# Kernel tuning notes

Measured on AMD Instinct MI355X. Metric: run time of the kernel, lower is better.

The kernel has to match this reference:

```python
import jax, jax.numpy as jnp
import numpy as np

N_NODES = 100000
N_EDGES = 1600000
F_IN = 128
HID = 128
N_GRAPHS = 64


def setup_inputs() -> dict:
    key = jax.random.key(0)
    ks = jax.random.split(key, 8)
    s = 1.0 / np.sqrt(HID)
    x = jax.random.normal(ks[0], (N_NODES, F_IN), jnp.float32)
    edge_index = jax.random.randint(ks[1], (2, N_EDGES), 0, N_NODES)
    batch = jnp.sort(jax.random.randint(ks[2], (N_NODES,), 0, N_GRAPHS))
    return {
        "x": x,
        "edge_index": edge_index,
        "batch": batch,
        "W1": jax.random.normal(ks[3], (F_IN, HID), jnp.float32) * s,
        "b1": jnp.zeros((HID,), jnp.float32),
        "W2": jax.random.normal(ks[4], (HID, HID), jnp.float32) * s,
        "b2": jnp.zeros((HID,), jnp.float32),
        "W3": jax.random.normal(ks[5], (HID, HID), jnp.float32) * s,
        "b3": jnp.zeros((HID,), jnp.float32),
        "lin_w": jax.random.normal(ks[6], (HID, 1), jnp.float32) * s,
        "lin_b": jnp.zeros((1,), jnp.float32),
    }


def reference(x, edge_index, batch, W1, b1, W2, b2, W3, b3, lin_w, lin_b):
    N = x.shape[0]
    # GCN normalization with self-loops: D^-1/2 (A+I) D^-1/2, computed once
    loops = jnp.arange(N)
    row = jnp.concatenate([edge_index[0], loops])  # source nodes
    col = jnp.concatenate([edge_index[1], loops])  # target nodes
    deg = jax.ops.segment_sum(jnp.ones_like(col, x.dtype), col, num_segments=N)
    dinv = jnp.where(deg > 0, jax.lax.rsqrt(deg), 0.0)
    norm = dinv[row] * dinv[col]  # [E+N]

    def conv(h, W, b):
        h = h @ W                                   # [N, H] linear transform
        msg = norm[:, None] * h[row]                # gather + scale [E+N, H]
        agg = jax.ops.segment_sum(msg, col, num_segments=N)
        return jax.nn.relu(agg + b)                 # dropout is identity in eval

    h = conv(x, W1, b1)
    h = conv(h, W2, b2)
    h = conv(h, W3, b3)

    # global mean pool per graph
    cnt = jax.ops.segment_sum(jnp.ones((N,), x.dtype), batch, num_segments=N_GRAPHS)
    pooled = jax.ops.segment_sum(h, batch, num_segments=N_GRAPHS) / jnp.maximum(cnt, 1.0)[:, None]
    out = pooled @ lin_w + lin_b  # [G, 1]
    return out.reshape(-1)
```

## Files before the change

### kernel.cpp

```cpp
#include <hip/hip_runtime.h>


typedef __attribute__((ext_vector_type(4))) float f32x4;
typedef __attribute__((ext_vector_type(8))) _Float16 half8;


__device__ __forceinline__ void gemm_f32_body(const float* __restrict__ H,
                                              const _Float16* __restrict__ W16,
                                              const float* __restrict__ dinv,
                                              _Float16* __restrict__ T16,
                                              int N, int bid) {
    const int tid = threadIdx.x;
    const int wv = tid >> 6;
    const int lane = tid & 63;
    const int r0 = bid * 64 + wv * 16;
    const int mrow = lane & 15;
    const int kq = lane >> 4;
    const int grow = r0 + mrow;
    const bool rok = grow < N;

    f32x4 acc[8];
    #pragma unroll
    for (int t = 0; t < 8; ++t) acc[t] = (f32x4){0.f, 0.f, 0.f, 0.f};

    #pragma unroll
    for (int c = 0; c < 4; ++c) {
        half8 a = (half8)(_Float16)0;
        if (rok) {
            const f32x4* Hp = (const f32x4*)(H + (size_t)grow * 128 + c * 32 + kq * 8);
            f32x4 a0 = __builtin_nontemporal_load(Hp);
            f32x4 a1 = __builtin_nontemporal_load(Hp + 1);
            a[0] = (_Float16)a0[0]; a[1] = (_Float16)a0[1];
            a[2] = (_Float16)a0[2]; a[3] = (_Float16)a0[3];
            a[4] = (_Float16)a1[0]; a[5] = (_Float16)a1[1];
            a[6] = (_Float16)a1[2]; a[7] = (_Float16)a1[3];
        }
        #pragma unroll
        for (int t = 0; t < 8; ++t) {
            half8 w = *(const half8*)&W16[(((c * 8 + t) * 64) + lane) * 8];
            acc[t] = __builtin_amdgcn_mfma_f32_16x16x32_f16(a, w, acc[t], 0, 0, 0);
        }
    }
    #pragma unroll
    for (int r = 0; r < 4; ++r) {
        int orow = r0 + kq * 4 + r;
        if (orow < N) {
            float dv = dinv[orow];
            half8 o;
            #pragma unroll
            for (int t = 0; t < 8; ++t) o[t] = (_Float16)(acc[t][r] * dv);
            *(half8*)(T16 + (size_t)orow * 128 + mrow * 8) = o;
        }
    }
}

__global__ __launch_bounds__(256) void prep_kernel(const float* __restrict__ W1,
                                                   const float* __restrict__ W2,
                                                   const float* __restrict__ W3,
                                                   const float* __restrict__ b1,
                                                   const float* __restrict__ b2,
                                                   const float* __restrict__ b3,
                                                   const float* __restrict__ lin_w,
                                                   _Float16* __restrict__ W16,
                                                   float* __restrict__ bperm,
                                                   const int* __restrict__ ei,
                                                   int* __restrict__ bucketCursor,
                                                   int* __restrict__ coarse,
                                                   int E, int N, int cap) {
    __shared__ int hist[256];
    __shared__ int base_s[256];
    __shared__ int lcur[256];
    if (blockIdx.x < 192) {
        int layer = blockIdx.x >> 6;
        const float* W = (layer == 0) ? W1 : (layer == 1) ? W2 : W3;
        _Float16* Wd = W16 + layer * 16384;
        int i = (blockIdx.x & 63) * 256 + threadIdx.x;
        int j = i & 7;
        int l = (i >> 3) & 63;
        int t = (i >> 9) & 7;
        int c = i >> 12;
        int k = c * 32 + (l >> 4) * 8 + j;
        int ksrc = (layer == 0) ? k : ((k & 7) * 16 + (k >> 3));
        int n = t * 16 + (l & 15);
        Wd[i] = (_Float16)W[ksrc * 128 + n];
    } else if (blockIdx.x < 200) {
        int a = blockIdx.x - 192;
        if (a < 4 && threadIdx.x < 128) {
            const float* src = (a == 0) ? b1 : (a == 1) ? b2 : (a == 2) ? b3 : lin_w;
            int p2 = threadIdx.x;
            bperm[a * 128 + p2] = src[(p2 & 7) * 16 + (p2 >> 3)];
        }
    } else {
        const int tid = threadIdx.x;
        const int nb = (N + 511) >> 9;
        for (int i = tid; i < nb; i += 256) { hist[i] = 0; lcur[i] = 0; }
        __syncthreads();
        const int e0 = (blockIdx.x - 200) * 2048 + tid * 8;
        int c[8], r[8];
        if (e0 < E && ((E & 3) == 0) && e0 + 7 < E) {
            int4 cA = *(const int4*)&ei[E + e0];
            int4 cB = *(const int4*)&ei[E + e0 + 4];
            int4 rA = *(const int4*)&ei[e0];
            int4 rB = *(const int4*)&ei[e0 + 4];
            c[0] = cA.x; c[1] = cA.y; c[2] = cA.z; c[3] = cA.w;
            c[4] = cB.x; c[5] = cB.y; c[6] = cB.z; c[7] = cB.w;
            r[0] = rA.x; r[1] = rA.y; r[2] = rA.z; r[3] = rA.w;
            r[4] = rB.x; r[5] = rB.y; r[6] = rB.z; r[7] = rB.w;
        } else {
            #pragma unroll
            for (int j = 0; j < 8; ++j) {
                int e = e0 + j;
                c[j] = (e < E) ? ei[E + e] : -1;
                r[j] = (e < E) ? ei[e] : 0;
            }
        }
        #pragma unroll
        for (int j = 0; j < 8; ++j)
            if (c[j] >= 0) atomicAdd(&hist[c[j] >> 9], 1);
        __syncthreads();
        for (int i = tid; i < nb; i += 256) {
            int h = hist[i];
            base_s[i] = h ? atomicAdd(&bucketCursor[i], h) : 0;
        }
        __syncthreads();
        #pragma unroll
        for (int j = 0; j < 8; ++j) {
            if (c[j] >= 0) {
                int b = c[j] >> 9;
                int pos = base_s[b] + atomicAdd(&lcur[b], 1);
                if (pos < cap)
                    coarse[(size_t)b * cap + pos] =
                        (int)(((unsigned)(c[j] & 511) << 23) | (unsigned)r[j]);
            }
        }
    }
}

__global__ __launch_bounds__(256) void bscan_kernel(int* __restrict__ bucketCursor,
                                                    int* __restrict__ bucketStart,
                                                    int* __restrict__ rowptr,
                                                    int nb, int cap, int N) {
    __shared__ int ts[256];
    const int t = threadIdx.x;
    int v = (t < nb) ? min(bucketCursor[t], cap) : 0;
    ts[t] = v;
    __syncthreads();
    for (int off = 1; off < 256; off <<= 1) {
        int add = (t >= off) ? ts[t - off] : 0;
        __syncthreads();
        ts[t] += add;
        __syncthreads();
    }
    if (t < nb) {
        bucketStart[t] = ts[t] - v;
        bucketCursor[t] = v;
    }
    if (t == nb - 1) rowptr[N] = ts[t];
}

__global__ __launch_bounds__(512) void binfill_kernel(const int* __restrict__ bucketStart,
                                                      const int* __restrict__ bucketCount,
                                                      const int* __restrict__ coarse,
                                                      int* __restrict__ rowptr,
                                                      float* __restrict__ dinv,
                                                      int* __restrict__ edges,
                                                      int N, int cap) {
    const int b = blockIdx.x;
    const int bn = b << 9;
    const int t = threadIdx.x;
    __shared__ int hist[512];
    __shared__ int scn[512];
    const int cnt = bucketCount[b];
    const size_t cbase = (size_t)b * cap;
    hist[t] = 0;
    __syncthreads();
    for (int i = t; i < cnt; i += 512)
        atomicAdd(&hist[((unsigned)coarse[cbase + i]) >> 23], 1);
    __syncthreads();
    const int myCnt = hist[t];
    if (bn + t < N) dinv[bn + t] = 1.0f / sqrtf((float)myCnt + 1.0f);
    scn[t] = myCnt;
    __syncthreads();
    for (int off = 1; off < 512; off <<= 1) {
        int add = (t >= off) ? scn[t - off] : 0;
        __syncthreads();
        scn[t] += add;
        __syncthreads();
    }
    const int rstart = bucketStart[b] + scn[t] - myCnt;
    if (bn + t < N) rowptr[bn + t] = rstart;
    hist[t] = rstart;
    __syncthreads();
    for (int i = t; i < cnt; i += 512) {
        int pk = coarse[cbase + i];
        int slot = atomicAdd(&hist[((unsigned)pk) >> 23], 1);
        edges[slot] = pk & 0x7FFFFF;
    }
}

__global__ __launch_bounds__(256) void gemm1_kernel(const float* __restrict__ x,
                                                    const _Float16* __restrict__ W16,
                                                    const float* __restrict__ dinv,
                                                    _Float16* __restrict__ A16, int N) {
    gemm_f32_body(x, W16, dinv, A16, N, blockIdx.x);
}

__global__ __launch_bounds__(256) void gemm_f16_kernel(const _Float16* __restrict__ H16,
                                                       const _Float16* __restrict__ W16,
                                                       const float* __restrict__ dinv,
                                                       _Float16* __restrict__ T16,
                                                       int N) {
    const int tid = threadIdx.x;
    const int wv = tid >> 6;
    const int lane = tid & 63;
    const int r0 = blockIdx.x * 64 + wv * 16;
    const int mrow = lane & 15;
    const int kq = lane >> 4;
    const int grow = r0 + mrow;
    const bool rok = grow < N;

    f32x4 acc[8];
    #pragma unroll
    for (int t = 0; t < 8; ++t) acc[t] = (f32x4){0.f, 0.f, 0.f, 0.f};

    #pragma unroll
    for (int c = 0; c < 4; ++c) {
        half8 a = (half8)(_Float16)0;
        if (rok) a = *(const half8*)(H16 + (size_t)grow * 128 + c * 32 + kq * 8);
        #pragma unroll
        for (int t = 0; t < 8; ++t) {
            half8 w = *(const half8*)&W16[(((c * 8 + t) * 64) + lane) * 8];
            acc[t] = __builtin_amdgcn_mfma_f32_16x16x32_f16(a, w, acc[t], 0, 0, 0);
        }
    }
    #pragma unroll
    for (int r = 0; r < 4; ++r) {
        int orow = r0 + kq * 4 + r;
        if (orow < N) {
            float dv = dinv[orow];
            half8 o;
            #pragma unroll
            for (int t = 0; t < 8; ++t) o[t] = (_Float16)(acc[t][r] * dv);
            *(half8*)(T16 + (size_t)orow * 128 + mrow * 8) = o;
        }
    }
}

__global__ __launch_bounds__(256) void agg_kernel(const int* __restrict__ rowptr,
                                                  const int* __restrict__ edges,
                                                  const float* __restrict__ dinv,
                                                  const _Float16* __restrict__ A16,
                                                  const float* __restrict__ bias,
                                                  _Float16* __restrict__ H16, int N) {
    int w = (blockIdx.x * 256 + threadIdx.x) >> 6;
    if (w >= N) return;
    const int lane = threadIdx.x & 63;
    const int g = lane >> 4;
    const int q = lane & 15;
    const int beg = rowptr[w];
    const int end = rowptr[w + 1];
    const float dn = dinv[w];
    const half8* A8 = (const half8*)A16;

    int myid = (beg + lane < end) ? edges[beg + lane] : 0;
    half8 sv = (half8)(_Float16)0;
    if (g == 0) sv = A8[(size_t)w * 16 + q];

    float a0 = 0.f, a1 = 0.f, a2 = 0.f, a3 = 0.f;
    float a4 = 0.f, a5 = 0.f, a6 = 0.f, a7 = 0.f;
    for (int base = beg; base < end; base += 16) {
        const int rr = base - beg + g;
        const bool v0 = base + g < end;
        const bool v1 = base + g + 4 < end;
        const bool v2 = base + g + 8 < end;
        const bool v3 = base + g + 12 < end;
        int s0 = __shfl(myid, rr < 64 ? rr : 63);
        int s1 = __shfl(myid, rr + 4 < 64 ? rr + 4 : 63);
        int s2 = __shfl(myid, rr + 8 < 64 ? rr + 8 : 63);
        int s3 = __shfl(myid, rr + 12 < 64 ? rr + 12 : 63);
        if (rr >= 64 && v0) s0 = edges[base + g];
        if (rr + 4 >= 64 && v1) s1 = edges[base + g + 4];
        if (rr + 8 >= 64 && v2) s2 = edges[base + g + 8];
        if (rr + 12 >= 64 && v3) s3 = edges[base + g + 12];
        half8 p0, p1, p2, p3;
        if (v0) p0 = A8[(size_t)s0 * 16 + q];
        if (v1) p1 = A8[(size_t)s1 * 16 + q];
        if (v2) p2 = A8[(size_t)s2 * 16 + q];
        if (v3) p3 = A8[(size_t)s3 * 16 + q];
        if (v0) {
            a0 += (float)p0[0]; a1 += (float)p0[1]; a2 += (float)p0[2]; a3 += (float)p0[3];
            a4 += (float)p0[4]; a5 += (float)p0[5]; a6 += (float)p0[6]; a7 += (float)p0[7];
        }
        if (v1) {
            a0 += (float)p1[0]; a1 += (float)p1[1]; a2 += (float)p1[2]; a3 += (float)p1[3];
            a4 += (float)p1[4]; a5 += (float)p1[5]; a6 += (float)p1[6]; a7 += (float)p1[7];
        }
        if (v2) {
            a0 += (float)p2[0]; a1 += (float)p2[1]; a2 += (float)p2[2]; a3 += (float)p2[3];
            a4 += (float)p2[4]; a5 += (float)p2[5]; a6 += (float)p2[6]; a7 += (float)p2[7];
        }
        if (v3) {
            a0 += (float)p3[0]; a1 += (float)p3[1]; a2 += (float)p3[2]; a3 += (float)p3[3];
            a4 += (float)p3[4]; a5 += (float)p3[5]; a6 += (float)p3[6]; a7 += (float)p3[7];
        }
    }
    a0 += __shfl_xor(a0, 16); a1 += __shfl_xor(a1, 16);
    a2 += __shfl_xor(a2, 16); a3 += __shfl_xor(a3, 16);
    a4 += __shfl_xor(a4, 16); a5 += __shfl_xor(a5, 16);
    a6 += __shfl_xor(a6, 16); a7 += __shfl_xor(a7, 16);
    a0 += __shfl_xor(a0, 32); a1 += __shfl_xor(a1, 32);
    a2 += __shfl_xor(a2, 32); a3 += __shfl_xor(a3, 32);
    a4 += __shfl_xor(a4, 32); a5 += __shfl_xor(a5, 32);
    a6 += __shfl_xor(a6, 32); a7 += __shfl_xor(a7, 32);

    if (g == 0) {
        float4 b0 = ((const float4*)bias)[q * 2];
        float4 b1 = ((const float4*)bias)[q * 2 + 1];
        half8 o;
        o[0] = (_Float16)fmaxf(fmaf(dn, a0 + (float)sv[0], b0.x), 0.f);
        o[1] = (_Float16)fmaxf(fmaf(dn, a1 + (float)sv[1], b0.y), 0.f);
        o[2] = (_Float16)fmaxf(fmaf(dn, a2 + (float)sv[2], b0.z), 0.f);
        o[3] = (_Float16)fmaxf(fmaf(dn, a3 + (float)sv[3], b0.w), 0.f);
        o[4] = (_Float16)fmaxf(fmaf(dn, a4 + (float)sv[4], b1.x), 0.f);
        o[5] = (_Float16)fmaxf(fmaf(dn, a5 + (float)sv[5], b1.y), 0.f);
        o[6] = (_Float16)fmaxf(fmaf(dn, a6 + (float)sv[6], b1.z), 0.f);
        o[7] = (_Float16)fmaxf(fmaf(dn, a7 + (float)sv[7], b1.w), 0.f);
        ((half8*)H16)[(size_t)w * 16 + q] = o;
    }
}

__global__ __launch_bounds__(256) void agg_head_kernel(const int* __restrict__ rowptr,
                                                       const int* __restrict__ edges,
                                                       const float* __restrict__ dinv,
                                                       const _Float16* __restrict__ A16,
                                                       const float* __restrict__ bias,
                                                       const float* __restrict__ lin_w,
                                                       float* __restrict__ nodeval, int N) {
    int w = (blockIdx.x * 256 + threadIdx.x) >> 6;
    if (w >= N) return;
    const int lane = threadIdx.x & 63;
    const int g = lane >> 4;
    const int q = lane & 15;
    const int beg = rowptr[w];
    const int end = rowptr[w + 1];
    const float dn = dinv[w];
    const half8* A8 = (const half8*)A16;

    int myid = (beg + lane < end) ? edges[beg + lane] : 0;
    half8 sv = (half8)(_Float16)0;
    if (g == 0) sv = A8[(size_t)w * 16 + q];

    float a0 = 0.f, a1 = 0.f, a2 = 0.f, a3 = 0.f;
    float a4 = 0.f, a5 = 0.f, a6 = 0.f, a7 = 0.f;
    for (int base = beg; base < end; base += 16) {
        const int rr = base - beg + g;
        const bool v0 = base + g < end;
        const bool v1 = base + g + 4 < end;
        const bool v2 = base + g + 8 < end;
        const bool v3 = base + g + 12 < end;
        int s0 = __shfl(myid, rr < 64 ? rr : 63);
        int s1 = __shfl(myid, rr + 4 < 64 ? rr + 4 : 63);
        int s2 = __shfl(myid, rr + 8 < 64 ? rr + 8 : 63);
        int s3 = __shfl(myid, rr + 12 < 64 ? rr + 12 : 63);
        if (rr >= 64 && v0) s0 = edges[base + g];
        if (rr + 4 >= 64 && v1) s1 = edges[base + g + 4];
        if (rr + 8 >= 64 && v2) s2 = edges[base + g + 8];
        if (rr + 12 >= 64 && v3) s3 = edges[base + g + 12];
        half8 p0, p1, p2, p3;
        if (v0) p0 = A8[(size_t)s0 * 16 + q];
        if (v1) p1 = A8[(size_t)s1 * 16 + q];
        if (v2) p2 = A8[(size_t)s2 * 16 + q];
        if (v3) p3 = A8[(size_t)s3 * 16 + q];
        if (v0) {
            a0 += (float)p0[0]; a1 += (float)p0[1]; a2 += (float)p0[2]; a3 += (float)p0[3];
            a4 += (float)p0[4]; a5 += (float)p0[5]; a6 += (float)p0[6]; a7 += (float)p0[7];
        }
        if (v1) {
            a0 += (float)p1[0]; a1 += (float)p1[1]; a2 += (float)p1[2]; a3 += (float)p1[3];
            a4 += (float)p1[4]; a5 += (float)p1[5]; a6 += (float)p1[6]; a7 += (float)p1[7];
        }
        if (v2) {
            a0 += (float)p2[0]; a1 += (float)p2[1]; a2 += (float)p2[2]; a3 += (float)p2[3];
            a4 += (float)p2[4]; a5 += (float)p2[5]; a6 += (float)p2[6]; a7 += (float)p2[7];
        }
        if (v3) {
            a0 += (float)p3[0]; a1 += (float)p3[1]; a2 += (float)p3[2]; a3 += (float)p3[3];
            a4 += (float)p3[4]; a5 += (float)p3[5]; a6 += (float)p3[6]; a7 += (float)p3[7];
        }
    }
    a0 += __shfl_xor(a0, 16); a1 += __shfl_xor(a1, 16);
    a2 += __shfl_xor(a2, 16); a3 += __shfl_xor(a3, 16);
    a4 += __shfl_xor(a4, 16); a5 += __shfl_xor(a5, 16);
    a6 += __shfl_xor(a6, 16); a7 += __shfl_xor(a7, 16);
    a0 += __shfl_xor(a0, 32); a1 += __shfl_xor(a1, 32);
    a2 += __shfl_xor(a2, 32); a3 += __shfl_xor(a3, 32);
    a4 += __shfl_xor(a4, 32); a5 += __shfl_xor(a5, 32);
    a6 += __shfl_xor(a6, 32); a7 += __shfl_xor(a7, 32);

    if (g == 0) {
        float4 b0 = ((const float4*)bias)[q * 2];
        float4 b1 = ((const float4*)bias)[q * 2 + 1];
        float4 w0 = ((const float4*)lin_w)[q * 2];
        float4 w1 = ((const float4*)lin_w)[q * 2 + 1];
        a0 = fmaf(dn, a0 + (float)sv[0], b0.x);
        a1 = fmaf(dn, a1 + (float)sv[1], b0.y);
        a2 = fmaf(dn, a2 + (float)sv[2], b0.z);
        a3 = fmaf(dn, a3 + (float)sv[3], b0.w);
        a4 = fmaf(dn, a4 + (float)sv[4], b1.x);
        a5 = fmaf(dn, a5 + (float)sv[5], b1.y);
        a6 = fmaf(dn, a6 + (float)sv[6], b1.z);
        a7 = fmaf(dn, a7 + (float)sv[7], b1.w);
        float s = fmaxf(a0, 0.f) * w0.x + fmaxf(a1, 0.f) * w0.y
                + fmaxf(a2, 0.f) * w0.z + fmaxf(a3, 0.f) * w0.w
                + fmaxf(a4, 0.f) * w1.x + fmaxf(a5, 0.f) * w1.y
                + fmaxf(a6, 0.f) * w1.z + fmaxf(a7, 0.f) * w1.w;
        s += __shfl_xor(s, 1);
        s += __shfl_xor(s, 2);
        s += __shfl_xor(s, 4);
        s += __shfl_xor(s, 8);
        if (q == 0) nodeval[w] = s;
    }
}

__device__ __forceinline__ int lower_bound_dev(const int* __restrict__ a, int n, int key) {
    int lo = 0, hi = n;
    while (lo < hi) {
        int mid = (lo + hi) >> 1;
        if (a[mid] < key) lo = mid + 1; else hi = mid;
    }
    return lo;
}

__global__ __launch_bounds__(256) void segreduce_kernel(const float* __restrict__ nodeval,
                                                        const int* __restrict__ batch,
                                                        const float* __restrict__ lin_b,
                                                        float* __restrict__ out, int N) {
    const int g = blockIdx.x;
    const int lo = lower_bound_dev(batch, N, g);
    const int hi = lower_bound_dev(batch, N, g + 1);
    float acc = 0.f;
    for (int n = lo + threadIdx.x; n < hi; n += 256) acc += nodeval[n];
    __shared__ float red[256];
    red[threadIdx.x] = acc;
    __syncthreads();
    for (int s = 128; s > 0; s >>= 1) {
        if (threadIdx.x < s) red[threadIdx.x] += red[threadIdx.x + s];
        __syncthreads();
    }
    if (threadIdx.x == 0) {
        float cnt = (float)(hi - lo);
        out[g] = red[0] / fmaxf(cnt, 1.0f) + lin_b[0];
    }
}

extern "C" void kernel_launch(void* const* d_in, const int* in_sizes, int n_in,
                              void* d_out, int out_size, void* d_ws, size_t ws_size,
                              hipStream_t stream) {
    const float* x     = (const float*)d_in[0];
    const int*   ei    = (const int*)d_in[1];
    const int*   batch = (const int*)d_in[2];
    const float* W1    = (const float*)d_in[3];
    const float* b1    = (const float*)d_in[4];
    const float* W2    = (const float*)d_in[5];
    const float* b2    = (const float*)d_in[6];
    const float* W3    = (const float*)d_in[7];
    const float* b3    = (const float*)d_in[8];
    const float* lin_w = (const float*)d_in[9];
    const float* lin_b = (const float*)d_in[10];
    float* out = (float*)d_out;

    const int N = in_sizes[0] / 128;
    const int E = in_sizes[1] / 2;
    const int nb = (N + 511) >> 9;
    const int cap = (((E + nb - 1) / nb) + 4096 + 3) & ~3;
    const int fBlocks = (E + 2047) / 2048;
    const int gBlocks = (N + 63) / 64;
    const int aBlocks = ((size_t)N * 64 + 255) / 256;

    _Float16* A16    = (_Float16*)d_ws;
    _Float16* H16    = A16 + (size_t)N * 128;
    float* dinv      = (float*)(H16 + (size_t)N * 128);
    int*   rowptr    = (int*)(dinv + N);
    int*   edges     = rowptr + (((size_t)N + 4) & ~(size_t)3);
    int*   coarse    = edges + (((size_t)E + 3) & ~(size_t)3);
    int*   bucketCursor = coarse + (size_t)nb * cap;
    int*   bucketStart  = bucketCursor + 256;
    float* nodeval   = (float*)(bucketStart + 256);
    _Float16* W16    = (_Float16*)(nodeval + N);
    float* bperm     = (float*)(W16 + 3 * 16384);

    hipMemsetAsync(bucketCursor, 0, (size_t)nb * sizeof(int), stream);
    prep_kernel<<<200 + fBlocks, 256, 0, stream>>>(W1, W2, W3, b1, b2, b3, lin_w,
                                                   W16, bperm, ei,
                                                   bucketCursor, coarse, E, N, cap);
    bscan_kernel<<<1, 256, 0, stream>>>(bucketCursor, bucketStart, rowptr, nb, cap, N);
    binfill_kernel<<<nb, 512, 0, stream>>>(bucketStart, bucketCursor, coarse,
                                           rowptr, dinv, edges, N, cap);
    gemm1_kernel<<<gBlocks, 256, 0, stream>>>(x, W16, dinv, A16, N);

    agg_kernel<<<aBlocks, 256, 0, stream>>>(rowptr, edges, dinv, A16, bperm, H16, N);
    gemm_f16_kernel<<<gBlocks, 256, 0, stream>>>(H16, W16 + 16384, dinv, A16, N);
    agg_kernel<<<aBlocks, 256, 0, stream>>>(rowptr, edges, dinv, A16, bperm + 128, H16, N);
    gemm_f16_kernel<<<gBlocks, 256, 0, stream>>>(H16, W16 + 32768, dinv, A16, N);
    agg_head_kernel<<<aBlocks, 256, 0, stream>>>(rowptr, edges, dinv,
                                                 A16, bperm + 256, bperm + 384, nodeval, N);
    segreduce_kernel<<<64, 256, 0, stream>>>(nodeval, batch, lin_b, out, N);
}
```

Measured before the change: 413.2 us.

## Process multiple nodes per wave in aggregation kernels with edge-id prefetch

Result: slower. 439.6 us (+6.4%).

```diff
diff --git a/kernel.cpp b/kernel.cpp
--- a/kernel.cpp
+++ b/kernel.cpp
@@ -3,6 +3,8 @@
 
 typedef __attribute__((ext_vector_type(4))) float f32x4;
 typedef __attribute__((ext_vector_type(8))) _Float16 half8;
+
+#define CNODES 8
 
 
 __device__ __forceinline__ void gemm_f32_body(const float* __restrict__ H,
@@ -252,80 +254,95 @@
                                                   const _Float16* __restrict__ A16,
                                                   const float* __restrict__ bias,
                                                   _Float16* __restrict__ H16, int N) {
-    int w = (blockIdx.x * 256 + threadIdx.x) >> 6;
-    if (w >= N) return;
+    const int wid = (blockIdx.x * 256 + threadIdx.x) >> 6;
+    const int a = wid * CNODES;
+    if (a >= N) return;
     const int lane = threadIdx.x & 63;
     const int g = lane >> 4;
     const int q = lane & 15;
-    const int beg = rowptr[w];
-    const int end = rowptr[w + 1];
-    const float dn = dinv[w];
     const half8* A8 = (const half8*)A16;
 
-    int myid = (beg + lane < end) ? edges[beg + lane] : 0;
-    half8 sv = (half8)(_Float16)0;
-    if (g == 0) sv = A8[(size_t)w * 16 + q];
-
-    float a0 = 0.f, a1 = 0.f, a2 = 0.f, a3 = 0.f;
-    float a4 = 0.f, a5 = 0.f, a6 = 0.f, a7 = 0.f;
-    for (int base = beg; base < end; base += 16) {
-        const int rr = base - beg + g;
-        const bool v0 = base + g < end;
-        const bool v1 = base + g + 4 < end;
-        const bool v2 = base + g + 8 < end;
-        const bool v3 = base + g + 12 < end;
-        int s0 = __shfl(myid, rr < 64 ? rr : 63);
-        int s1 = __shfl(myid, rr + 4 < 64 ? rr + 4 : 63);
-        int s2 = __shfl(myid, rr + 8 < 64 ? rr + 8 : 63);
-        int s3 = __shfl(myid, rr + 12 < 64 ? rr + 12 : 63);
-        if (rr >= 64 && v0) s0 = edges[base + g];
-        if (rr + 4 >= 64 && v1) s1 = edges[base + g + 4];
-        if (rr + 8 >= 64 && v2) s2 = edges[base + g + 8];
-        if (rr + 12 >= 64 && v3) s3 = edges[base + g + 12];
-        half8 p0, p1, p2, p3;
-        if (v0) p0 = A8[(size_t)s0 * 16 + q];
-        if (v1) p1 = A8[(size_t)s1 * 16 + q];
-        if (v2) p2 = A8[(size_t)s2 * 16 + q];
-        if (v3) p3 = A8[(size_t)s3 * 16 + q];
-        if (v0) {
-            a0 += (float)p0[0]; a1 += (float)p0[1]; a2 += (float)p0[2]; a3 += (float)p0[3];
-            a4 += (float)p0[4]; a5 += (float)p0[5]; a6 += (float)p0[6]; a7 += (float)p0[7];
-        }
-        if (v1) {
-            a0 += (float)p1[0]; a1 += (float)p1[1]; a2 += (float)p1[2]; a3 += (float)p1[3];
-            a4 += (float)p1[4]; a5 += (float)p1[5]; a6 += (float)p1[6]; a7 += (float)p1[7];
-        }
-        if (v2) {
-            a0 += (float)p2[0]; a1 += (float)p2[1]; a2 += (float)p2[2]; a3 += (float)p2[3];
-            a4 += (float)p2[4]; a5 += (float)p2[5]; a6 += (float)p2[6]; a7 += (float)p2[7];
-        }
-        if (v3) {
-            a0 += (float)p3[0]; a1 += (float)p3[1]; a2 += (float)p3[2]; a3 += (float)p3[3];
-            a4 += (float)p3[4]; a5 += (float)p3[5]; a6 += (float)p3[6]; a7 += (float)p3[7];
-        }
-    }
-    a0 += __shfl_xor(a0, 16); a1 += __shfl_xor(a1, 16);
-    a2 += __shfl_xor(a2, 16); a3 += __shfl_xor(a3, 16);
-    a4 += __shfl_xor(a4, 16); a5 += __shfl_xor(a5, 16);
-    a6 += __shfl_xor(a6, 16); a7 += __shfl_xor(a7, 16);
-    a0 += __shfl_xor(a0, 32); a1 += __shfl_xor(a1, 32);
-    a2 += __shfl_xor(a2, 32); a3 += __shfl_xor(a3, 32);
-    a4 += __shfl_xor(a4, 32); a5 += __shfl_xor(a5, 32);
-    a6 += __shfl_xor(a6, 32); a7 += __shfl_xor(a7, 32);
-
-    if (g == 0) {
-        float4 b0 = ((const float4*)bias)[q * 2];
-        float4 b1 = ((const float4*)bias)[q * 2 + 1];
-        half8 o;
-        o[0] = (_Float16)fmaxf(fmaf(dn, a0 + (float)sv[0], b0.x), 0.f);
-        o[1] = (_Float16)fmaxf(fmaf(dn, a1 + (float)sv[1], b0.y), 0.f);
-        o[2] = (_Float16)fmaxf(fmaf(dn, a2 + (float)sv[2], b0.z), 0.f);
-        o[3] = (_Float16)fmaxf(fmaf(dn, a3 + (float)sv[3], b0.w), 0.f);
-        o[4] = (_Float16)fmaxf(fmaf(dn, a4 + (float)sv[4], b1.x), 0.f);
-        o[5] = (_Float16)fmaxf(fmaf(dn, a5 + (float)sv[5], b1.y), 0.f);
-        o[6] = (_Float16)fmaxf(fmaf(dn, a6 + (float)sv[6], b1.z), 0.f);
-        o[7] = (_Float16)fmaxf(fmaf(dn, a7 + (float)sv[7], b1.w), 0.f);
-        ((half8*)H16)[(size_t)w * 16 + q] = o;
+    int rpl = rowptr[min(a + min(lane, CNODES), N)];
+    float4 bv0 = ((const float4*)bias)[q * 2];
+    float4 bv1 = ((const float4*)bias)[q * 2 + 1];
+
+    int beg = __shfl(rpl, 0);
+    int end = __shfl(rpl, 1);
+    int ids = (beg + lane < end) ? edges[beg + lane] : 0;
+
+    #pragma unroll 1
+    for (int i = 0; i < CNODES; ++i) {
+        const int n = a + i;
+        if (n >= N) break;
+        const int begN = end;
+        const int endN = __shfl(rpl, min(i + 2, CNODES));
+        int idsN = 0;
+        if (i + 1 < CNODES && n + 1 < N && begN + lane < endN)
+            idsN = edges[begN + lane];
+        half8 sv = (half8)(_Float16)0;
+        if (g == 0) sv = A8[(size_t)n * 16 + q];
+
+        float a0 = 0.f, a1 = 0.f, a2 = 0.f, a3 = 0.f;
+        float a4 = 0.f, a5 = 0.f, a6 = 0.f, a7 = 0.f;
+        for (int base = beg; base < end; base += 16) {
+            const int rr = base - beg + g;
+            const bool v0 = base + g < end;
+            const bool v1 = base + g + 4 < end;
+            const bool v2 = base + g + 8 < end;
+            const bool v3 = base + g + 12 < end;
+            int s0 = __shfl(ids, rr < 64 ? rr : 63);
+            int s1 = __shfl(ids, rr + 4 < 64 ? rr + 4 : 63);
+            int s2 = __shfl(ids, rr + 8 < 64 ? rr + 8 : 63);
+            int s3 = __shfl(ids, rr + 12 < 64 ? rr + 12 : 63);
+            if (rr >= 64 && v0) s0 = edges[base + g];
+            if (rr + 4 >= 64 && v1) s1 = edges[base + g + 4];
+            if (rr + 8 >= 64 && v2) s2 = edges[base + g + 8];
+            if (rr + 12 >= 64 && v3) s3 = edges[base + g + 12];
+            half8 p0, p1, p2, p3;
+            if (v0) p0 = A8[(size_t)s0 * 16 + q];
+            if (v1) p1 = A8[(size_t)s1 * 16 + q];
+            if (v2) p2 = A8[(size_t)s2 * 16 + q];
+            if (v3) p3 = A8[(size_t)s3 * 16 + q];
+            if (v0) {
+                a0 += (float)p0[0]; a1 += (float)p0[1]; a2 += (float)p0[2]; a3 += (float)p0[3];
+                a4 += (float)p0[4]; a5 += (float)p0[5]; a6 += (float)p0[6]; a7 += (float)p0[7];
+            }
+            if (v1) {
+                a0 += (float)p1[0]; a1 += (float)p1[1]; a2 += (float)p1[2]; a3 += (float)p1[3];
+                a4 += (float)p1[4]; a5 += (float)p1[5]; a6 += (float)p1[6]; a7 += (float)p1[7];
+            }
+            if (v2) {
+                a0 += (float)p2[0]; a1 += (float)p2[1]; a2 += (float)p2[2]; a3 += (float)p2[3];
+                a4 += (float)p2[4]; a5 += (float)p2[5]; a6 += (float)p2[6]; a7 += (float)p2[7];
+            }
+            if (v3) {
+                a0 += (float)p3[0]; a1 += (float)p3[1]; a2 += (float)p3[2]; a3 += (float)p3[3];
+                a4 += (float)p3[4]; a5 += (float)p3[5]; a6 += (float)p3[6]; a7 += (float)p3[7];
+            }
+        }
+        a0 += __shfl_xor(a0, 16); a1 += __shfl_xor(a1, 16);
+        a2 += __shfl_xor(a2, 16); a3 += __shfl_xor(a3, 16);
+        a4 += __shfl_xor(a4, 16); a5 += __shfl_xor(a5, 16);
+        a6 += __shfl_xor(a6, 16); a7 += __shfl_xor(a7, 16);
+        a0 += __shfl_xor(a0, 32); a1 += __shfl_xor(a1, 32);
+        a2 += __shfl_xor(a2, 32); a3 += __shfl_xor(a3, 32);
+        a4 += __shfl_xor(a4, 32); a5 += __shfl_xor(a5, 32);
+        a6 += __shfl_xor(a6, 32); a7 += __shfl_xor(a7, 32);
+
+        if (g == 0) {
+            const float dn = dinv[n];
+            half8 o;
+            o[0] = (_Float16)fmaxf(fmaf(dn, a0 + (float)sv[0], bv0.x), 0.f);
+            o[1] = (_Float16)fmaxf(fmaf(dn, a1 + (float)sv[1], bv0.y), 0.f);
+            o[2] = (_Float16)fmaxf(fmaf(dn, a2 + (float)sv[2], bv0.z), 0.f);
+            o[3] = (_Float16)fmaxf(fmaf(dn, a3 + (float)sv[3], bv0.w), 0.f);
+            o[4] = (_Float16)fmaxf(fmaf(dn, a4 + (float)sv[4], bv1.x), 0.f);
+            o[5] = (_Float16)fmaxf(fmaf(dn, a5 + (float)sv[5], bv1.y), 0.f);
+            o[6] = (_Float16)fmaxf(fmaf(dn, a6 + (float)sv[6], bv1.z), 0.f);
+            o[7] = (_Float16)fmaxf(fmaf(dn, a7 + (float)sv[7], bv1.w), 0.f);
+            ((half8*)H16)[(size_t)n * 16 + q] = o;
+        }
+        beg = begN; end = endN; ids = idsN;
     }
 }
 
@@ -336,89 +353,104 @@
                                                        const float* __restrict__ bias,
                                                        const float* __restrict__ lin_w,
                                                        float* __restrict__ nodeval, int N) {
-    int w = (blockIdx.x * 256 + threadIdx.x) >> 6;
-    if (w >= N) return;
+    const int wid = (blockIdx.x * 256 + threadIdx.x) >> 6;
+    const int a = wid * CNODES;
+    if (a >= N) return;
     const int lane = threadIdx.x & 63;
     const int g = lane >> 4;
     const int q = lane & 15;
-    const int beg = rowptr[w];
-    const int end = rowptr[w + 1];
-    const float dn = dinv[w];
     const half8* A8 = (const half8*)A16;
 
-    int myid = (beg + lane < end) ? edges[beg + lane] : 0;
-    half8 sv = (half8)(_Float16)0;
-    if (g == 0) sv = A8[(size_t)w * 16 + q];
-
-    float a0 = 0.f, a1 = 0.f, a2 = 0.f, a3 = 0.f;
-    float a4 = 0.f, a5 = 0.f, a6 = 0.f, a7 = 0.f;
-    for (int base = beg; base < end; base += 16) {
-        const int rr = base - beg + g;
-        const bool v0 = base + g < end;
-        const bool v1 = base + g + 4 < end;
-        const bool v2 = base + g + 8 < end;
-        const bool v3 = base + g + 12 < end;
-        int s0 = __shfl(myid, rr < 64 ? rr : 63);
-        int s1 = __shfl(myid, rr + 4 < 64 ? rr + 4 : 63);
-        int s2 = __shfl(myid, rr + 8 < 64 ? rr + 8 : 63);
-        int s3 = __shfl(myid, rr + 12 < 64 ? rr + 12 : 63);
-        if (rr >= 64 && v0) s0 = edges[base + g];
-        if (rr + 4 >= 64 && v1) s1 = edges[base + g + 4];
-        if (rr + 8 >= 64 && v2) s2 = edges[base + g + 8];
-        if (rr + 12 >= 64 && v3) s3 = edges[base + g + 12];
-        half8 p0, p1, p2, p3;
-        if (v0) p0 = A8[(size_t)s0 * 16 + q];
-        if (v1) p1 = A8[(size_t)s1 * 16 + q];
-        if (v2) p2 = A8[(size_t)s2 * 16 + q];
-        if (v3) p3 = A8[(size_t)s3 * 16 + q];
-        if (v0) {
-            a0 += (float)p0[0]; a1 += (float)p0[1]; a2 += (float)p0[2]; a3 += (float)p0[3];
-            a4 += (float)p0[4]; a5 += (float)p0[5]; a6 += (float)p0[6]; a7 += (float)p0[7];
-        }
-        if (v1) {
-            a0 += (float)p1[0]; a1 += (float)p1[1]; a2 += (float)p1[2]; a3 += (float)p1[3];
-            a4 += (float)p1[4]; a5 += (float)p1[5]; a6 += (float)p1[6]; a7 += (float)p1[7];
-        }
-        if (v2) {
-            a0 += (float)p2[0]; a1 += (float)p2[1]; a2 += (float)p2[2]; a3 += (float)p2[3];
-            a4 += (float)p2[4]; a5 += (float)p2[5]; a6 += (float)p2[6]; a7 += (float)p2[7];
-        }
-        if (v3) {
-            a0 += (float)p3[0]; a1 += (float)p3[1]; a2 += (float)p3[2]; a3 += (float)p3[3];
-            a4 += (float)p3[4]; a5 += (float)p3[5]; a6 += (float)p3[6]; a7 += (float)p3[7];
-        }
-    }
-    a0 += __shfl_xor(a0, 16); a1 += __shfl_xor(a1, 16);
-    a2 += __shfl_xor(a2, 16); a3 += __shfl_xor(a3, 16);
-    a4 += __shfl_xor(a4, 16); a5 += __shfl_xor(a5, 16);
-    a6 += __shfl_xor(a6, 16); a7 += __shfl_xor(a7, 16);
-    a0 += __shfl_xor(a0, 32); a1 += __shfl_xor(a1, 32);
-    a2 += __shfl_xor(a2, 32); a3 += __shfl_xor(a3, 32);
-    a4 += __shfl_xor(a4, 32); a5 += __shfl_xor(a5, 32);
-    a6 += __shfl_xor(a6, 32); a7 += __shfl_xor(a7, 32);
-
-    if (g == 0) {
-        float4 b0 = ((const float4*)bias)[q * 2];
-        float4 b1 = ((const float4*)bias)[q * 2 + 1];
-        float4 w0 = ((const float4*)lin_w)[q * 2];
-        float4 w1 = ((const float4*)lin_w)[q * 2 + 1];
-        a0 = fmaf(dn, a0 + (float)sv[0], b0.x);
-        a1 = fmaf(dn, a1 + (float)sv[1], b0.y);
-        a2 = fmaf(dn, a2 + (float)sv[2], b0.z);
-        a3 = fmaf(dn, a3 + (float)sv[3], b0.w);
-        a4 = fmaf(dn, a4 + (float)sv[4], b1.x);
-        a5 = fmaf(dn, a5 + (float)sv[5], b1.y);
-        a6 = fmaf(dn, a6 + (float)sv[6], b1.z);
-        a7 = fmaf(dn, a7 + (float)sv[7], b1.w);
-        float s = fmaxf(a0, 0.f) * w0.x + fmaxf(a1, 0.f) * w0.y
-                + fmaxf(a2, 0.f) * w0.z + fmaxf(a3, 0.f) * w0.w
-                + fmaxf(a4, 0.f) * w1.x + fmaxf(a5, 0.f) * w1.y
-                + fmaxf(a6, 0.f) * w1.z + fmaxf(a7, 0.f) * w1.w;
-        s += __shfl_xor(s, 1);
-        s += __shfl_xor(s, 2);
-        s += __shfl_xor(s, 4);
-        s += __shfl_xor(s, 8);
-        if (q == 0) nodeval[w] = s;
+    int rpl = rowptr[min(a + min(lane, CNODES), N)];
+    float4 bv0 = ((const float4*)bias)[q * 2];
+    float4 bv1 = ((const float4*)bias)[q * 2 + 1];
+    float4 w0 = ((const float4*)lin_w)[q * 2];
+    float4 w1 = ((const float4*)lin_w)[q * 2 + 1];
+
+    int beg = __shfl(rpl, 0);
+    int end = __shfl(rpl, 1);
+    int ids = (beg + lane < end) ? edges[beg + lane] : 0;
+
+    #pragma unroll 1
+    for (int i = 0; i < CNODES; ++i) {
+        const int n = a + i;
+        if (n >= N) break;
+        const int begN = end;
+        const int endN = __shfl(rpl, min(i + 2, CNODES));
+        int idsN = 0;
+        if (i + 1 < CNODES && n + 1 < N && begN + lane < endN)
+            idsN = edges[begN + lane];
+        half8 sv = (half8)(_Float16)0;
+        if (g == 0) sv = A8[(size_t)n * 16 + q];
+
+        float a0 = 0.f, a1 = 0.f, a2 = 0.f, a3 = 0.f;
+        float a4 = 0.f, a5 = 0.f, a6 = 0.f, a7 = 0.f;
+        for (int base = beg; base < end; base += 16) {
+            const int rr = base - beg + g;
+            const bool v0 = base + g < end;
+            const bool v1 = base + g + 4 < end;
+            const bool v2 = base + g + 8 < end;
+            const bool v3 = base + g + 12 < end;
+            int s0 = __shfl(ids, rr < 64 ? rr : 63);
+            int s1 = __shfl(ids, rr + 4 < 64 ? rr + 4 : 63);
+            int s2 = __shfl(ids, rr + 8 < 64 ? rr + 8 : 63);
+            int s3 = __shfl(ids, rr + 12 < 64 ? rr + 12 : 63);
+            if (rr >= 64 && v0) s0 = edges[base + g];
+            if (rr + 4 >= 64 && v1) s1 = edges[base + g + 4];
+            if (rr + 8 >= 64 && v2) s2 = edges[base + g + 8];
+            if (rr + 12 >= 64 && v3) s3 = edges[base + g + 12];
+            half8 p0, p1, p2, p3;
+            if (v0) p0 = A8[(size_t)s0 * 16 + q];
+            if (v1) p1 = A8[(size_t)s1 * 16 + q];
+            if (v2) p2 = A8[(size_t)s2 * 16 + q];
+            if (v3) p3 = A8[(size_t)s3 * 16 + q];
+            if (v0) {
+                a0 += (float)p0[0]; a1 += (float)p0[1]; a2 += (float)p0[2]; a3 += (float)p0[3];
+                a4 += (float)p0[4]; a5 += (float)p0[5]; a6 += (float)p0[6]; a7 += (float)p0[7];
+            }
+            if (v1) {
+                a0 += (float)p1[0]; a1 += (float)p1[1]; a2 += (float)p1[2]; a3 += (float)p1[3];
+                a4 += (float)p1[4]; a5 += (float)p1[5]; a6 += (float)p1[6]; a7 += (float)p1[7];
+            }
+            if (v2) {
+                a0 += (float)p2[0]; a1 += (float)p2[1]; a2 += (float)p2[2]; a3 += (float)p2[3];
+                a4 += (float)p2[4]; a5 += (float)p2[5]; a6 += (float)p2[6]; a7 += (float)p2[7];
+            }
+            if (v3) {
+                a0 += (float)p3[0]; a1 += (float)p3[1]; a2 += (float)p3[2]; a3 += (float)p3[3];
+                a4 += (float)p3[4]; a5 += (float)p3[5]; a6 += (float)p3[6]; a7 += (float)p3[7];
+            }
+        }
+        a0 += __shfl_xor(a0, 16); a1 += __shfl_xor(a1, 16);
+        a2 += __shfl_xor(a2, 16); a3 += __shfl_xor(a3, 16);
+        a4 += __shfl_xor(a4, 16); a5 += __shfl_xor(a5, 16);
+        a6 += __shfl_xor(a6, 16); a7 += __shfl_xor(a7, 16);
+        a0 += __shfl_xor(a0, 32); a1 += __shfl_xor(a1, 32);
+        a2 += __shfl_xor(a2, 32); a3 += __shfl_xor(a3, 32);
+        a4 += __shfl_xor(a4, 32); a5 += __shfl_xor(a5, 32);
+        a6 += __shfl_xor(a6, 32); a7 += __shfl_xor(a7, 32);
+
+        if (g == 0) {
+            const float dn = dinv[n];
+            float r0 = fmaf(dn, a0 + (float)sv[0], bv0.x);
+            float r1 = fmaf(dn, a1 + (float)sv[1], bv0.y);
+            float r2 = fmaf(dn, a2 + (float)sv[2], bv0.z);
+            float r3 = fmaf(dn, a3 + (float)sv[3], bv0.w);
+            float r4 = fmaf(dn, a4 + (float)sv[4], bv1.x);
+            float r5 = fmaf(dn, a5 + (float)sv[5], bv1.y);
+            float r6 = fmaf(dn, a6 + (float)sv[6], bv1.z);
+            float r7 = fmaf(dn, a7 + (float)sv[7], bv1.w);
+            float s = fmaxf(r0, 0.f) * w0.x + fmaxf(r1, 0.f) * w0.y
+                    + fmaxf(r2, 0.f) * w0.z + fmaxf(r3, 0.f) * w0.w
+                    + fmaxf(r4, 0.f) * w1.x + fmaxf(r5, 0.f) * w1.y
+                    + fmaxf(r6, 0.f) * w1.z + fmaxf(r7, 0.f) * w1.w;
+            s += __shfl_xor(s, 1);
+            s += __shfl_xor(s, 2);
+            s += __shfl_xor(s, 4);
+            s += __shfl_xor(s, 8);
+            if (q == 0) nodeval[n] = s;
+        }
+        beg = begN; end = endN; ids = idsN;
     }
 }
 
@@ -475,7 +507,8 @@
     const int cap = (((E + nb - 1) / nb) + 4096 + 3) & ~3;
     const int fBlocks = (E + 2047) / 2048;
     const int gBlocks = (N + 63) / 64;
-    const int aBlocks = ((size_t)N * 64 + 255) / 256;
+    const int nWaves = (N + CNODES - 1) / CNODES;
+    const int aBlocks = ((size_t)nWaves * 64 + 255) / 256;
 
     _Float16* A16    = (_Float16*)d_ws;
     _Float16* H16    = A16 + (size_t)N * 128;
```
